# Optimization experiments

Hardware: AMD Instinct MI355X
Metric: run time of the kernel (lower is better)

## Reference

```python
import jax, jax.numpy as jnp
import numpy as np

EMBED_DIM = 1024
NUM_HEADS = 16
D_K = EMBED_DIM // NUM_HEADS


def setup_inputs() -> dict:
    key = jax.random.key(0)
    ks = jax.random.split(key, 9)
    s = 1.0 / np.sqrt(EMBED_DIM)
    x = jax.random.normal(ks[0], (4, 2048, EMBED_DIM), dtype=jnp.float32)
    # nn.Linear weights stored as [out, in]; we keep [in, out] for x @ W
    W_q = jax.random.uniform(ks[1], (EMBED_DIM, EMBED_DIM), jnp.float32, -s, s)
    b_q = jax.random.uniform(ks[2], (EMBED_DIM,), jnp.float32, -s, s)
    W_k = jax.random.uniform(ks[3], (EMBED_DIM, EMBED_DIM), jnp.float32, -s, s)
    b_k = jax.random.uniform(ks[4], (EMBED_DIM,), jnp.float32, -s, s)
    W_v = jax.random.uniform(ks[5], (EMBED_DIM, EMBED_DIM), jnp.float32, -s, s)
    b_v = jax.random.uniform(ks[6], (EMBED_DIM,), jnp.float32, -s, s)
    W_o = jax.random.uniform(ks[7], (EMBED_DIM, EMBED_DIM), jnp.float32, -s, s)
    b_o = jax.random.uniform(ks[8], (EMBED_DIM,), jnp.float32, -s, s)
    return {"x": x, "W_q": W_q, "b_q": b_q, "W_k": W_k, "b_k": b_k,
            "W_v": W_v, "b_v": b_v, "W_o": W_o, "b_o": b_o}


def reference(x, W_q, b_q, W_k, b_k, W_v, b_v, W_o, b_o):
    B, N, _ = x.shape
    # QKV projections, split into heads: [B, H, N, d_k]
    def proj(W, b):
        return (x @ W + b).reshape(B, N, NUM_HEADS, D_K).transpose(0, 2, 1, 3)
    Q, K, V = proj(W_q, b_q), proj(W_k, b_k), proj(W_v, b_v)
    scale = 1.0 / np.sqrt(D_K).astype(np.float32)
    scores = jnp.einsum('bhqd,bhkd->bhqk', Q, K) * scale  # [B,H,N,N]
    weights = jax.nn.softmax(scores, axis=-1)
    # dropout is identity in eval mode
    attn = jnp.einsum('bhqk,bhkd->bhqd', weights, V)  # [B,H,N,d_k]
    attn = attn.transpose(0, 2, 1, 3).reshape(B, N, EMBED_DIM)
    return attn @ W_o + b_o
```

## Files before the change

kernel.cpp:

```cpp
#include <hip/hip_runtime.h>

typedef __bf16 bf16;
typedef __attribute__((ext_vector_type(8))) __bf16 bf16x8;
typedef __attribute__((ext_vector_type(4))) __bf16 bf16x4;
typedef __attribute__((ext_vector_type(4))) float f32x4;

static __device__ __forceinline__ f32x4 mfma16(bf16x8 a, bf16x8 b, f32x4 c) {
    return __builtin_amdgcn_mfma_f32_16x16x32_bf16(a, b, c, 0, 0, 0);
}

static __device__ __forceinline__ void gll16(const bf16* g, bf16* l) {
    __builtin_amdgcn_global_load_lds(
        (const __attribute__((address_space(1))) unsigned int*)g,
        (__attribute__((address_space(3))) unsigned int*)l, 16, 0, 0);
}

__global__ __launch_bounds__(256) void prep_kernel(
    const float* __restrict__ x, bf16* __restrict__ xb,
    const float* __restrict__ Wq, const float* __restrict__ Wk,
    const float* __restrict__ Wv, const float* __restrict__ Wo,
    bf16* __restrict__ WTqkv, bf16* __restrict__ WTo,
    const float* __restrict__ bq, const float* __restrict__ bk,
    const float* __restrict__ bv, float* __restrict__ bcat)
{
    __shared__ bf16 tile[64][65];
    const int bid = blockIdx.x;
    const int tid = threadIdx.x;

    if (bid < 4096) {
        size_t i = ((size_t)bid * 256 + tid) * 8;
        float4 a0 = *(const float4*)&x[i];
        float4 a1 = *(const float4*)&x[i + 4];
        bf16x8 v = {(bf16)a0.x, (bf16)a0.y, (bf16)a0.z, (bf16)a0.w,
                    (bf16)a1.x, (bf16)a1.y, (bf16)a1.z, (bf16)a1.w};
        *(bf16x8*)&xb[i] = v;
    } else if (bid < 5120) {
        const int wb = bid - 4096;
        const int mi = wb >> 8;
        const int t  = wb & 255;
        const int tr = t >> 4;
        const int tc = t & 15;
        const float* src = (mi == 0) ? Wq : (mi == 1) ? Wk : (mi == 2) ? Wv : Wo;
        bf16* dst = (mi < 3) ? (WTqkv + (size_t)mi * 1024 * 1024) : WTo;

        #pragma unroll
        for (int i = 0; i < 16; i++) {
            int idx = i * 256 + tid;
            int rl = idx >> 6, cl = idx & 63;
            tile[rl][cl] = (bf16)src[(size_t)(tr * 64 + rl) * 1024 + tc * 64 + cl];
        }
        __syncthreads();
        #pragma unroll
        for (int i = 0; i < 16; i++) {
            int idx = i * 256 + tid;
            int rl = idx >> 6, cl = idx & 63;
            dst[(size_t)(tc * 64 + rl) * 1024 + tr * 64 + cl] = tile[cl][rl];
        }
    } else {
        int i = (bid - 5120) * 256 + tid;
        if (i < 1024) bcat[i] = bq[i];
        else if (i < 2048) bcat[i] = bk[i - 1024];
        else if (i < 3072) bcat[i] = bv[i - 2048];
    }
}

#define QSCALE 0.18033688011112043f
__global__ __launch_bounds__(256) void gemm_bf16_kernel(
    const bf16* __restrict__ A, const bf16* __restrict__ BT,
    const float* __restrict__ bias, bf16* __restrict__ C,
    int M, int N, int K, int scaleQ)
{
    __shared__ bf16 sA[2][128 * 32];
    __shared__ bf16 sB[2][128 * 32];
    const int tid  = threadIdx.x;
    const int lane = tid & 63;
    const int wave = tid >> 6;
    const int quad = lane >> 4;
    const int l15  = lane & 15;
    const int wm = (wave >> 1) * 64;
    const int wn = (wave & 1) * 64;
    const int m0 = blockIdx.y * 128;
    const int n0 = blockIdx.x * 128;

    const f32x4 fzero = {0.f, 0.f, 0.f, 0.f};
    f32x4 acc[4][4];
    #pragma unroll
    for (int i = 0; i < 4; i++)
        #pragma unroll
        for (int j = 0; j < 4; j++) acc[i][j] = fzero;

    float bv[4];
    #pragma unroll
    for (int nc = 0; nc < 4; nc++) bv[nc] = bias[n0 + wn + nc * 16 + l15];

    const int rA = lane >> 2;
    const int cAsw = ((lane & 3) ^ ((lane >> 3) & 3)) * 8;
    const int gsw = (l15 >> 1) & 3;

#define GSTAGE(K0, BUF)                                                           \
    _Pragma("unroll")                                                             \
    for (int p = 0; p < 2; p++) {                                                 \
        int r16 = (wave * 2 + p) * 16;                                            \
        gll16(&A[(size_t)(m0 + r16 + rA) * K + (K0) + cAsw], &sA[BUF][r16 * 32]); \
        gll16(&BT[(size_t)(n0 + r16 + rA) * K + (K0) + cAsw], &sB[BUF][r16 * 32]);\
    }

#define GCOMPUTE(BUF)                                                             \
    {                                                                             \
        bf16x8 aF[4], bF[4];                                                      \
        _Pragma("unroll")                                                         \
        for (int mc = 0; mc < 4; mc++)                                            \
            aF[mc] = *(const bf16x8*)&sA[BUF][(wm + mc * 16 + l15) * 32 + ((quad ^ gsw) * 8)]; \
        _Pragma("unroll")                                                         \
        for (int nc = 0; nc < 4; nc++)                                            \
            bF[nc] = *(const bf16x8*)&sB[BUF][(wn + nc * 16 + l15) * 32 + ((quad ^ gsw) * 8)]; \
        _Pragma("unroll")                                                         \
        for (int mc = 0; mc < 4; mc++)                                            \
            _Pragma("unroll")                                                     \
            for (int nc = 0; nc < 4; nc++)                                        \
                acc[mc][nc] = mfma16(aF[mc], bF[nc], acc[mc][nc]);                \
    }

    GSTAGE(0, 0);
    __syncthreads();
    int buf = 0;
    for (int k0 = 0; k0 < K - 32; k0 += 32, buf ^= 1) {
        GSTAGE(k0 + 32, buf ^ 1);
        __builtin_amdgcn_sched_barrier(0);
        GCOMPUTE(buf);
        __syncthreads();
    }
    GCOMPUTE(buf);

    const float sc = (scaleQ && n0 < 1024) ? QSCALE : 1.0f;
    #pragma unroll
    for (int mc = 0; mc < 4; mc++) {
        #pragma unroll
        for (int reg = 0; reg < 4; reg++) {
            int row = m0 + wm + mc * 16 + quad * 4 + reg;
            size_t base = (size_t)row * N + n0 + wn;
            #pragma unroll
            for (int nc = 0; nc < 4; nc++)
                C[base + nc * 16 + l15] = (bf16)((acc[mc][nc][reg] + bv[nc]) * sc);
        }
    }
}

__global__ __launch_bounds__(256) void gemm_bf16_f32out_kernel(
    const bf16* __restrict__ A, const bf16* __restrict__ BT,
    const float* __restrict__ bias, float* __restrict__ C,
    int M, int N, int K)
{
    __shared__ bf16 sA[2][128 * 32];
    __shared__ bf16 sB[2][128 * 32];
    const int tid  = threadIdx.x;
    const int lane = tid & 63;
    const int wave = tid >> 6;
    const int quad = lane >> 4;
    const int l15  = lane & 15;
    const int wm = (wave >> 1) * 64;
    const int wn = (wave & 1) * 64;
    const int m0 = blockIdx.y * 128;
    const int n0 = blockIdx.x * 128;

    const f32x4 fzero = {0.f, 0.f, 0.f, 0.f};
    f32x4 acc[4][4];
    #pragma unroll
    for (int i = 0; i < 4; i++)
        #pragma unroll
        for (int j = 0; j < 4; j++) acc[i][j] = fzero;

    float bv[4];
    #pragma unroll
    for (int nc = 0; nc < 4; nc++) bv[nc] = bias[n0 + wn + nc * 16 + l15];

    const int rA = lane >> 2;
    const int cAsw = ((lane & 3) ^ ((lane >> 3) & 3)) * 8;
    const int gsw = (l15 >> 1) & 3;

    GSTAGE(0, 0);
    __syncthreads();
    int buf = 0;
    for (int k0 = 0; k0 < K - 32; k0 += 32, buf ^= 1) {
        GSTAGE(k0 + 32, buf ^ 1);
        __builtin_amdgcn_sched_barrier(0);
        GCOMPUTE(buf);
        __syncthreads();
    }
    GCOMPUTE(buf);

#undef GSTAGE
#undef GCOMPUTE

    #pragma unroll
    for (int mc = 0; mc < 4; mc++) {
        #pragma unroll
        for (int reg = 0; reg < 4; reg++) {
            int row = m0 + wm + mc * 16 + quad * 4 + reg;
            size_t base = (size_t)row * N + n0 + wn;
            #pragma unroll
            for (int nc = 0; nc < 4; nc++)
                C[base + nc * 16 + l15] = acc[mc][nc][reg] + bv[nc];
        }
    }
}

__global__ __launch_bounds__(256) void vtrans_kernel(
    const bf16* __restrict__ QKVp, bf16* __restrict__ Vt)
{
    __shared__ bf16 tile[64][65];
    const int bid = blockIdx.x;
    const int bh = bid >> 5;
    const int nt = bid & 31;
    const int b = bh >> 4, h = bh & 15;
    const int tid = threadIdx.x;

    #pragma unroll
    for (int i = 0; i < 16; i++) {
        int idx = i * 256 + tid;
        int rl = idx >> 6, cl = idx & 63;
        tile[rl][cl] = QKVp[(size_t)(b * 2048 + nt * 64 + rl) * 3072 + 2048 + h * 64 + cl];
    }
    __syncthreads();
    #pragma unroll
    for (int i = 0; i < 16; i++) {
        int idx = i * 256 + tid;
        int rl = idx >> 6, cl = idx & 63;
        Vt[((size_t)bh * 64 + rl) * 2048 + nt * 64 + cl] = tile[cl][rl];
    }
}

__global__ __launch_bounds__(128, 2) void attn_kernel(
    const bf16* __restrict__ QKV, const bf16* __restrict__ Vt,
    bf16* __restrict__ Opre)
{
    __shared__ bf16 sK[2][64 * 64];
    __shared__ bf16 sV[2][64 * 64];

    const int tid  = threadIdx.x;
    const int lane = tid & 63;
    const int w    = tid >> 6;
    const int quad = lane >> 4;
    const int l15  = lane & 15;
    const int bid = (blockIdx.x & 7) * 128 + (blockIdx.x >> 3);
    const int bh = bid >> 4;
    const int qt = bid & 15;
    const int b = bh >> 4, h = bh & 15;
    const int q0 = qt * 128;

    bf16x8 qF[4][2];
    #pragma unroll
    for (int g = 0; g < 4; g++) {
        size_t qrow = (size_t)(b * 2048 + q0 + w * 64 + g * 16 + l15) * 3072 + h * 64;
        qF[g][0] = *(const bf16x8*)&QKV[qrow + quad * 8];
        qF[g][1] = *(const bf16x8*)&QKV[qrow + 32 + quad * 8];
    }

    const f32x4 fzero = {0.f, 0.f, 0.f, 0.f};
    const bf16 one = (bf16)1.0f;
    const bf16x8 ones = {one, one, one, one, one, one, one, one};
    f32x4 ps[4] = {fzero, fzero, fzero, fzero};
    f32x4 o[4][4];
    #pragma unroll
    for (int g = 0; g < 4; g++)
        #pragma unroll
        for (int mt = 0; mt < 4; mt++) o[g][mt] = fzero;

    const int srow = tid >> 3, sseg = tid & 7;
    const size_t kbase = (size_t)(b * 2048) * 3072 + 1024 + h * 64;
    const size_t vbase = (size_t)bh * 64 * 2048;
    const int sgsw = sseg ^ ((srow & 3) | (((srow >> 3) & 1) << 2));

    const int swk = (l15 & 3) | (((l15 >> 2) & 1) << 2);
    const int swv = (l15 & 3) | (((l15 >> 3) & 1) << 2);

    bf16x8 stK[4], stV[4];

#define ISSUE(KEY0)                                                               \
    _Pragma("unroll")                                                             \
    for (int p = 0; p < 4; p++) {                                                 \
        int row = srow + p * 16;                                                  \
        stK[p] = *(const bf16x8*)&QKV[kbase + (size_t)((KEY0) + row) * 3072 + sseg * 8]; \
        stV[p] = *(const bf16x8*)&Vt[vbase + (size_t)row * 2048 + (KEY0) + sseg * 8];    \
    }

#define COMMIT(BUF)                                                               \
    _Pragma("unroll")                                                             \
    for (int p = 0; p < 4; p++) {                                                 \
        int row = srow + p * 16;                                                  \
        *(bf16x8*)&sK[BUF][row * 64 + sgsw * 8] = stK[p];                         \
        *(bf16x8*)&sV[BUF][row * 64 + sgsw * 8] = stV[p];                         \
    }

    auto compute_tile = [&](const bf16* sKc, const bf16* sVc) {
        bf16x8 pB[4][2];
        __builtin_amdgcn_s_setprio(1);
        #pragma unroll
        for (int c = 0; c < 2; c++) {
            int kr = ((l15 >> 2) << 3) + (c << 2) + (l15 & 3);
            bf16x8 kA0 = *(const bf16x8*)&sKc[kr * 64 + ((quad ^ swk) * 8)];
            bf16x8 kA1 = *(const bf16x8*)&sKc[kr * 64 + (((4 + quad) ^ swk) * 8)];
            #pragma unroll
            for (int g = 0; g < 4; g++) {
                f32x4 st = mfma16(kA0, qF[g][0], fzero);
                st = mfma16(kA1, qF[g][1], st);
                #pragma unroll
                for (int r = 0; r < 4; r++) {
                    float p = __builtin_amdgcn_exp2f(st[r]);
                    pB[g][0][c * 4 + r] = (bf16)p;
                }
            }
        }
        bf16x8 vA0[4];
        #pragma unroll
        for (int mt = 0; mt < 4; mt++)
            vA0[mt] = *(const bf16x8*)&sVc[(mt * 16 + l15) * 64 + ((quad ^ swv) * 8)];
        #pragma unroll
        for (int c = 0; c < 2; c++) {
            int kr = ((l15 >> 2) << 3) + (c << 2) + (l15 & 3) + 32;
            bf16x8 kA0 = *(const bf16x8*)&sKc[kr * 64 + ((quad ^ swk) * 8)];
            bf16x8 kA1 = *(const bf16x8*)&sKc[kr * 64 + (((4 + quad) ^ swk) * 8)];
            #pragma unroll
            for (int g = 0; g < 4; g++) {
                f32x4 st = mfma16(kA0, qF[g][0], fzero);
                st = mfma16(kA1, qF[g][1], st);
                #pragma unroll
                for (int r = 0; r < 4; r++) {
                    float p = __builtin_amdgcn_exp2f(st[r]);
                    pB[g][1][c * 4 + r] = (bf16)p;
                }
            }
        }
        #pragma unroll
        for (int g = 0; g < 4; g++) ps[g] = mfma16(ones, pB[g][0], ps[g]);
        #pragma unroll
        for (int mt = 0; mt < 4; mt++)
            #pragma unroll
            for (int g = 0; g < 4; g++)
                o[g][mt] = mfma16(vA0[mt], pB[g][0], o[g][mt]);
        bf16x8 vA1[4];
        #pragma unroll
        for (int mt = 0; mt < 4; mt++)
            vA1[mt] = *(const bf16x8*)&sVc[(mt * 16 + l15) * 64 + (((4 + quad) ^ swv) * 8)];
        #pragma unroll
        for (int g = 0; g < 4; g++) ps[g] = mfma16(ones, pB[g][1], ps[g]);
        #pragma unroll
        for (int mt = 0; mt < 4; mt++)
            #pragma unroll
            for (int g = 0; g < 4; g++)
                o[g][mt] = mfma16(vA1[mt], pB[g][1], o[g][mt]);
        __builtin_amdgcn_s_setprio(0);
    };

    ISSUE(0);
    COMMIT(0);
    __syncthreads();

    for (int t = 0; t < 31; t++) {
        ISSUE((t + 1) * 64);
        __builtin_amdgcn_sched_barrier(0);
        compute_tile(sK[t & 1], sV[t & 1]);
        COMMIT((t + 1) & 1);
        __syncthreads();
    }
    compute_tile(sK[1], sV[1]);

#undef ISSUE
#undef COMMIT

    #pragma unroll
    for (int g = 0; g < 4; g++) {
        float inv = 1.0f / ps[g][0];
        size_t obase = (size_t)(b * 2048 + q0 + w * 64 + g * 16 + l15) * 1024 + h * 64;
        #pragma unroll
        for (int mt = 0; mt < 4; mt++) {
            bf16x4 ov = {(bf16)(o[g][mt][0] * inv), (bf16)(o[g][mt][1] * inv),
                         (bf16)(o[g][mt][2] * inv), (bf16)(o[g][mt][3] * inv)};
            *(bf16x4*)&Opre[obase + mt * 16 + quad * 4] = ov;
        }
    }
}

extern "C" void kernel_launch(void* const* d_in, const int* in_sizes, int n_in,
                              void* d_out, int out_size, void* d_ws, size_t ws_size,
                              hipStream_t stream)
{
    const float* x  = (const float*)d_in[0];
    const float* Wq = (const float*)d_in[1];
    const float* bq = (const float*)d_in[2];
    const float* Wk = (const float*)d_in[3];
    const float* bk = (const float*)d_in[4];
    const float* Wv = (const float*)d_in[5];
    const float* bv = (const float*)d_in[6];
    const float* Wo = (const float*)d_in[7];
    const float* bo = (const float*)d_in[8];
    float* out = (float*)d_out;

    bf16* WTqkv = (bf16*)d_ws;
    bf16* WTo   = WTqkv + (size_t)3072 * 1024;
    float* bcat = (float*)(WTo + (size_t)1024 * 1024);
    bf16* QKVp  = (bf16*)(bcat + 4096);
    bf16* Vt    = QKVp + (size_t)8192 * 3072;
    bf16* Apre  = Vt + (size_t)64 * 64 * 2048;
    bf16* xb    = Apre;
    (void)ws_size; (void)n_in; (void)in_sizes; (void)out_size;

    prep_kernel<<<5132, 256, 0, stream>>>(x, xb, Wq, Wk, Wv, Wo, WTqkv, WTo,
                                          bq, bk, bv, bcat);
    gemm_bf16_kernel<<<dim3(24, 64), 256, 0, stream>>>(xb, WTqkv, bcat, QKVp, 8192, 3072, 1024, 1);
    vtrans_kernel<<<2048, 256, 0, stream>>>(QKVp, Vt);
    attn_kernel<<<1024, 128, 0, stream>>>(QKVp, Vt, Apre);
    gemm_bf16_f32out_kernel<<<dim3(8, 64), 256, 0, stream>>>(Apre, WTo, bo, out, 8192, 1024, 1024);
}
```

Baseline: 269.0 us.

## Software-pipeline QK^T and PV across tiles with direct global-to-LDS loads

```diff
diff --git a/kernel.cpp b/kernel.cpp
--- a/kernel.cpp
+++ b/kernel.cpp
@@ -274,99 +274,96 @@
     const int swk = (l15 & 3) | (((l15 >> 2) & 1) << 2);
     const int swv = (l15 & 3) | (((l15 >> 3) & 1) << 2);
 
-    bf16x8 stK[4], stV[4];
-
-#define ISSUE(KEY0)                                                               \
+    bf16x8 pAr[4][2], pBr[4][2];
+    bf16x8 vA[4][2];
+
+#define STAGE(KEY0, BUF)                                                          \
     _Pragma("unroll")                                                             \
     for (int p = 0; p < 4; p++) {                                                 \
         int row = srow + p * 16;                                                  \
-        stK[p] = *(const bf16x8*)&QKV[kbase + (size_t)((KEY0) + row) * 3072 + sseg * 8]; \
-        stV[p] = *(const bf16x8*)&Vt[vbase + (size_t)row * 2048 + (KEY0) + sseg * 8];    \
-    }
-
-#define COMMIT(BUF)                                                               \
-    _Pragma("unroll")                                                             \
-    for (int p = 0; p < 4; p++) {                                                 \
-        int row = srow + p * 16;                                                  \
-        *(bf16x8*)&sK[BUF][row * 64 + sgsw * 8] = stK[p];                         \
-        *(bf16x8*)&sV[BUF][row * 64 + sgsw * 8] = stV[p];                         \
-    }
-
-    auto compute_tile = [&](const bf16* sKc, const bf16* sVc) {
-        bf16x8 pB[4][2];
+        gll16(&QKV[kbase + (size_t)((KEY0) + row) * 3072 + sgsw * 8],             \
+              &sK[BUF][(w * 8 + p * 16) * 64]);                                   \
+        gll16(&Vt[vbase + (size_t)row * 2048 + (KEY0) + sgsw * 8],                \
+              &sV[BUF][(w * 8 + p * 16) * 64]);                                   \
+    }
+
+#define VREAD(SV)                                                                 \
+    _Pragma("unroll")                                                             \
+    for (int mt = 0; mt < 4; mt++) {                                              \
+        vA[mt][0] = *(const bf16x8*)&(SV)[(mt * 16 + l15) * 64 + ((quad ^ swv) * 8)];       \
+        vA[mt][1] = *(const bf16x8*)&(SV)[(mt * 16 + l15) * 64 + (((4 + quad) ^ swv) * 8)]; \
+    }
+
+#define QKT(PB, SK)                                                               \
+    _Pragma("unroll")                                                             \
+    for (int ch = 0; ch < 2; ch++) {                                              \
+        _Pragma("unroll")                                                         \
+        for (int c = 0; c < 2; c++) {                                             \
+            int kr = ((l15 >> 2) << 3) + (c << 2) + (l15 & 3) + ch * 32;          \
+            bf16x8 kA0 = *(const bf16x8*)&(SK)[kr * 64 + ((quad ^ swk) * 8)];     \
+            bf16x8 kA1 = *(const bf16x8*)&(SK)[kr * 64 + (((4 + quad) ^ swk) * 8)];\
+            _Pragma("unroll")                                                     \
+            for (int g = 0; g < 4; g++) {                                         \
+                f32x4 st = mfma16(kA0, qF[g][0], fzero);                          \
+                st = mfma16(kA1, qF[g][1], st);                                   \
+                _Pragma("unroll")                                                 \
+                for (int r = 0; r < 4; r++)                                       \
+                    PB[g][ch][c * 4 + r] = (bf16)__builtin_amdgcn_exp2f(st[r]);   \
+            }                                                                     \
+        }                                                                         \
+    }
+
+#define PVACC(PA)                                                                 \
+    _Pragma("unroll")                                                             \
+    for (int g = 0; g < 4; g++) {                                                 \
+        ps[g] = mfma16(ones, PA[g][0], ps[g]);                                    \
+        ps[g] = mfma16(ones, PA[g][1], ps[g]);                                    \
+    }                                                                             \
+    _Pragma("unroll")                                                             \
+    for (int mt = 0; mt < 4; mt++)                                                \
+        _Pragma("unroll")                                                         \
+        for (int g = 0; g < 4; g++) {                                             \
+            o[g][mt] = mfma16(vA[mt][0], PA[g][0], o[g][mt]);                     \
+            o[g][mt] = mfma16(vA[mt][1], PA[g][1], o[g][mt]);                     \
+        }
+
+    STAGE(0, 0);
+    __syncthreads();
+    QKT(pAr, sK[0]);
+    STAGE(64, 1);
+
+    for (int tt = 0; tt < 15; tt++) {
+        const int t = tt * 2;
+        VREAD(sV[0]);
+        __syncthreads();
+        STAGE((t + 2) * 64, 0);
+        __builtin_amdgcn_sched_barrier(0);
         __builtin_amdgcn_s_setprio(1);
-        #pragma unroll
-        for (int c = 0; c < 2; c++) {
-            int kr = ((l15 >> 2) << 3) + (c << 2) + (l15 & 3);
-            bf16x8 kA0 = *(const bf16x8*)&sKc[kr * 64 + ((quad ^ swk) * 8)];
-            bf16x8 kA1 = *(const bf16x8*)&sKc[kr * 64 + (((4 + quad) ^ swk) * 8)];
-            #pragma unroll
-            for (int g = 0; g < 4; g++) {
-                f32x4 st = mfma16(kA0, qF[g][0], fzero);
-                st = mfma16(kA1, qF[g][1], st);
-                #pragma unroll
-                for (int r = 0; r < 4; r++) {
-                    float p = __builtin_amdgcn_exp2f(st[r]);
-                    pB[g][0][c * 4 + r] = (bf16)p;
-                }
-            }
-        }
-        bf16x8 vA0[4];
-        #pragma unroll
-        for (int mt = 0; mt < 4; mt++)
-            vA0[mt] = *(const bf16x8*)&sVc[(mt * 16 + l15) * 64 + ((quad ^ swv) * 8)];
-        #pragma unroll
-        for (int c = 0; c < 2; c++) {
-            int kr = ((l15 >> 2) << 3) + (c << 2) + (l15 & 3) + 32;
-            bf16x8 kA0 = *(const bf16x8*)&sKc[kr * 64 + ((quad ^ swk) * 8)];
-            bf16x8 kA1 = *(const bf16x8*)&sKc[kr * 64 + (((4 + quad) ^ swk) * 8)];
-            #pragma unroll
-            for (int g = 0; g < 4; g++) {
-                f32x4 st = mfma16(kA0, qF[g][0], fzero);
-                st = mfma16(kA1, qF[g][1], st);
-                #pragma unroll
-                for (int r = 0; r < 4; r++) {
-                    float p = __builtin_amdgcn_exp2f(st[r]);
-                    pB[g][1][c * 4 + r] = (bf16)p;
-                }
-            }
-        }
-        #pragma unroll
-        for (int g = 0; g < 4; g++) ps[g] = mfma16(ones, pB[g][0], ps[g]);
-        #pragma unroll
-        for (int mt = 0; mt < 4; mt++)
-            #pragma unroll
-            for (int g = 0; g < 4; g++)
-                o[g][mt] = mfma16(vA0[mt], pB[g][0], o[g][mt]);
-        bf16x8 vA1[4];
-        #pragma unroll
-        for (int mt = 0; mt < 4; mt++)
-            vA1[mt] = *(const bf16x8*)&sVc[(mt * 16 + l15) * 64 + (((4 + quad) ^ swv) * 8)];
-        #pragma unroll
-        for (int g = 0; g < 4; g++) ps[g] = mfma16(ones, pB[g][1], ps[g]);
-        #pragma unroll
-        for (int mt = 0; mt < 4; mt++)
-            #pragma unroll
-            for (int g = 0; g < 4; g++)
-                o[g][mt] = mfma16(vA1[mt], pB[g][1], o[g][mt]);
+        QKT(pBr, sK[1]);
+        PVACC(pAr);
         __builtin_amdgcn_s_setprio(0);
-    };
-
-    ISSUE(0);
-    COMMIT(0);
+        VREAD(sV[1]);
+        __syncthreads();
+        STAGE((t + 3) * 64, 1);
+        __builtin_amdgcn_sched_barrier(0);
+        __builtin_amdgcn_s_setprio(1);
+        QKT(pAr, sK[0]);
+        PVACC(pBr);
+        __builtin_amdgcn_s_setprio(0);
+    }
+    VREAD(sV[0]);
     __syncthreads();
-
-    for (int t = 0; t < 31; t++) {
-        ISSUE((t + 1) * 64);
-        __builtin_amdgcn_sched_barrier(0);
-        compute_tile(sK[t & 1], sV[t & 1]);
-        COMMIT((t + 1) & 1);
-        __syncthreads();
-    }
-    compute_tile(sK[1], sV[1]);
-
-#undef ISSUE
-#undef COMMIT
+    __builtin_amdgcn_s_setprio(1);
+    QKT(pBr, sK[1]);
+    PVACC(pAr);
+    __builtin_amdgcn_s_setprio(0);
+    VREAD(sV[1]);
+    PVACC(pBr);
+
+#undef STAGE
+#undef VREAD
+#undef QKT
+#undef PVACC
 
     #pragma unroll
     for (int g = 0; g < 4; g++) {
```

After: 265.5 us. Within noise of the previous version (-1.3%).

## Rewrite QKV GEMM with 256-wide tiles, 8 waves, and fused V transpose

Applied to the files above, without the earlier changes.

```diff
diff --git a/kernel.cpp b/kernel.cpp
--- a/kernel.cpp
+++ b/kernel.cpp
@@ -65,22 +65,36 @@
 }
 
 #define QSCALE 0.18033688011112043f
-__global__ __launch_bounds__(256) void gemm_bf16_kernel(
+__global__ __launch_bounds__(512, 2) void gemm_qkv_kernel(
     const bf16* __restrict__ A, const bf16* __restrict__ BT,
     const float* __restrict__ bias, bf16* __restrict__ C,
-    int M, int N, int K, int scaleQ)
+    bf16* __restrict__ Vt)
 {
-    __shared__ bf16 sA[2][128 * 32];
-    __shared__ bf16 sB[2][128 * 32];
+    __shared__ bf16 sA[2 * 8192];
+    __shared__ bf16 sB[2 * 16384];
+
     const int tid  = threadIdx.x;
     const int lane = tid & 63;
     const int wave = tid >> 6;
+    const int wm   = wave >> 2;
+    const int wn   = wave & 3;
     const int quad = lane >> 4;
     const int l15  = lane & 15;
-    const int wm = (wave >> 1) * 64;
-    const int wn = (wave & 1) * 64;
+    const int gx   = l15 & 7;
     const int m0 = blockIdx.y * 128;
-    const int n0 = blockIdx.x * 128;
+    const int n0 = blockIdx.x * 256;
+    const int K = 1024;
+    const int N = 3072;
+
+    const int srow8 = lane >> 3;
+    const int scol  = ((lane & 7) ^ srow8) * 8;
+
+#define S_A(L, T)                                                                  \
+    gll16(&A[(size_t)(m0 + (L) * 64 + wave * 8 + srow8) * K + (T) * 64 + scol],    \
+          &sA[((T) & 1) * 8192 + ((L) * 64 + wave * 8) * 64])
+#define S_B(L, T)                                                                  \
+    gll16(&BT[(size_t)(n0 + (L) * 64 + wave * 8 + srow8) * K + (T) * 64 + scol],   \
+          &sB[((T) & 1) * 16384 + ((L) * 64 + wave * 8) * 64])
 
     const f32x4 fzero = {0.f, 0.f, 0.f, 0.f};
     f32x4 acc[4][4];
@@ -91,57 +105,132 @@
 
     float bv[4];
     #pragma unroll
-    for (int nc = 0; nc < 4; nc++) bv[nc] = bias[n0 + wn + nc * 16 + l15];
-
-    const int rA = lane >> 2;
-    const int cAsw = ((lane & 3) ^ ((lane >> 3) & 3)) * 8;
-    const int gsw = (l15 >> 1) & 3;
-
-#define GSTAGE(K0, BUF)                                                           \
-    _Pragma("unroll")                                                             \
-    for (int p = 0; p < 2; p++) {                                                 \
-        int r16 = (wave * 2 + p) * 16;                                            \
-        gll16(&A[(size_t)(m0 + r16 + rA) * K + (K0) + cAsw], &sA[BUF][r16 * 32]); \
-        gll16(&BT[(size_t)(n0 + r16 + rA) * K + (K0) + cAsw], &sB[BUF][r16 * 32]);\
-    }
-
-#define GCOMPUTE(BUF)                                                             \
-    {                                                                             \
-        bf16x8 aF[4], bF[4];                                                      \
-        _Pragma("unroll")                                                         \
-        for (int mc = 0; mc < 4; mc++)                                            \
-            aF[mc] = *(const bf16x8*)&sA[BUF][(wm + mc * 16 + l15) * 32 + ((quad ^ gsw) * 8)]; \
-        _Pragma("unroll")                                                         \
-        for (int nc = 0; nc < 4; nc++)                                            \
-            bF[nc] = *(const bf16x8*)&sB[BUF][(wn + nc * 16 + l15) * 32 + ((quad ^ gsw) * 8)]; \
-        _Pragma("unroll")                                                         \
-        for (int mc = 0; mc < 4; mc++)                                            \
-            _Pragma("unroll")                                                     \
-            for (int nc = 0; nc < 4; nc++)                                        \
-                acc[mc][nc] = mfma16(aF[mc], bF[nc], acc[mc][nc]);                \
-    }
-
-    GSTAGE(0, 0);
-    __syncthreads();
-    int buf = 0;
-    for (int k0 = 0; k0 < K - 32; k0 += 32, buf ^= 1) {
-        GSTAGE(k0 + 32, buf ^ 1);
+    for (int cf = 0; cf < 4; cf++) bv[cf] = bias[n0 + wn * 64 + cf * 16 + l15];
+
+    bf16x8 aF[4][2], bF[2][2];
+
+#define PH0(CB)                                                                    \
+    {                                                                              \
+        _Pragma("unroll")                                                          \
+        for (int mc = 0; mc < 4; mc++)                                             \
+            _Pragma("unroll")                                                      \
+            for (int ks = 0; ks < 2; ks++)                                         \
+                aF[mc][ks] = *(const bf16x8*)&sA[(CB) * 8192 +                     \
+                    (wm * 64 + mc * 16 + l15) * 64 + (((ks * 4 + quad) ^ gx) * 8)];\
+        _Pragma("unroll")                                                          \
+        for (int nc = 0; nc < 2; nc++)                                             \
+            _Pragma("unroll")                                                      \
+            for (int ks = 0; ks < 2; ks++)                                         \
+                bF[nc][ks] = *(const bf16x8*)&sB[(CB) * 16384 +                    \
+                    (wn * 64 + nc * 16 + l15) * 64 + (((ks * 4 + quad) ^ gx) * 8)];\
+        __builtin_amdgcn_s_barrier();                                              \
+        __builtin_amdgcn_s_setprio(1);                                             \
+        _Pragma("unroll")                                                          \
+        for (int mc = 0; mc < 4; mc++)                                             \
+            _Pragma("unroll")                                                      \
+            for (int nc = 0; nc < 2; nc++)                                         \
+                _Pragma("unroll")                                                  \
+                for (int ks = 0; ks < 2; ks++)                                     \
+                    acc[mc][nc] = mfma16(aF[mc][ks], bF[nc][ks], acc[mc][nc]);     \
+        __builtin_amdgcn_s_setprio(0);                                             \
+        __builtin_amdgcn_s_barrier();                                              \
+    }
+
+#define PH1(CB)                                                                    \
+    {                                                                              \
+        _Pragma("unroll")                                                          \
+        for (int nc = 0; nc < 2; nc++)                                             \
+            _Pragma("unroll")                                                      \
+            for (int ks = 0; ks < 2; ks++)                                         \
+                bF[nc][ks] = *(const bf16x8*)&sB[(CB) * 16384 +                    \
+                    (wn * 64 + 32 + nc * 16 + l15) * 64 +                          \
+                    (((ks * 4 + quad) ^ gx) * 8)];                                 \
+        __builtin_amdgcn_s_barrier();                                              \
+        __builtin_amdgcn_s_setprio(1);                                             \
+        _Pragma("unroll")                                                          \
+        for (int mc = 0; mc < 4; mc++)                                             \
+            _Pragma("unroll")                                                      \
+            for (int nc = 0; nc < 2; nc++)                                         \
+                _Pragma("unroll")                                                  \
+                for (int ks = 0; ks < 2; ks++)                                     \
+                    acc[mc][2 + nc] = mfma16(aF[mc][ks], bF[nc][ks], acc[mc][2 + nc]); \
+        __builtin_amdgcn_s_setprio(0);                                             \
+        __builtin_amdgcn_s_barrier();                                              \
+    }
+
+    S_A(0, 0); S_A(1, 0);
+    S_B(0, 0); S_B(1, 0); S_B(2, 0); S_B(3, 0);
+    S_A(0, 1); S_A(1, 1);
+    asm volatile("s_waitcnt vmcnt(2)" ::: "memory");
+    __builtin_amdgcn_s_barrier();
+
+    for (int i = 0; i < 14; ++i) {
+        const int cb = i & 1;
+        S_B(0, i + 1); S_B(1, i + 1);
         __builtin_amdgcn_sched_barrier(0);
-        GCOMPUTE(buf);
+        PH0(cb);
+        S_B(2, i + 1); S_B(3, i + 1);
+        __builtin_amdgcn_sched_barrier(0);
+        PH1(cb);
+        S_A(0, i + 2); S_A(1, i + 2);
+        asm volatile("s_waitcnt vmcnt(2)" ::: "memory");
+        __builtin_amdgcn_s_barrier();
+    }
+    S_B(0, 15); S_B(1, 15);
+    __builtin_amdgcn_sched_barrier(0);
+    PH0(0);
+    S_B(2, 15); S_B(3, 15);
+    __builtin_amdgcn_sched_barrier(0);
+    PH1(0);
+    asm volatile("s_waitcnt vmcnt(0)" ::: "memory");
+    __builtin_amdgcn_s_barrier();
+    PH0(1);
+    PH1(1);
+
+#undef S_A
+#undef S_B
+#undef PH0
+#undef PH1
+
+    if (n0 >= 2048) {
         __syncthreads();
-    }
-    GCOMPUTE(buf);
-
-    const float sc = (scaleQ && n0 < 1024) ? QSCALE : 1.0f;
-    #pragma unroll
-    for (int mc = 0; mc < 4; mc++) {
-        #pragma unroll
-        for (int reg = 0; reg < 4; reg++) {
-            int row = m0 + wm + mc * 16 + quad * 4 + reg;
-            size_t base = (size_t)row * N + n0 + wn;
-            #pragma unroll
-            for (int nc = 0; nc < 4; nc++)
-                C[base + nc * 16 + l15] = (bf16)((acc[mc][nc][reg] + bv[nc]) * sc);
+        #pragma unroll
+        for (int mc = 0; mc < 4; mc++)
+            #pragma unroll
+            for (int cf = 0; cf < 4; cf++) {
+                int col = wn * 64 + cf * 16 + l15;
+                int row = wm * 64 + mc * 16 + quad * 4;
+                bf16x4 v = {(bf16)(acc[mc][cf][0] + bv[cf]),
+                            (bf16)(acc[mc][cf][1] + bv[cf]),
+                            (bf16)(acc[mc][cf][2] + bv[cf]),
+                            (bf16)(acc[mc][cf][3] + bv[cf])};
+                *(bf16x4*)&sB[col * 128 + (row ^ ((col & 15) << 3))] = v;
+            }
+        __syncthreads();
+        const int b = m0 >> 11, mloc = m0 & 2047;
+        const int hp = (n0 - 2048) >> 6;
+        #pragma unroll
+        for (int it = 0; it < 16; it++) {
+            int chunk = it * 512 + tid;
+            int col = chunk >> 5;
+            int tok = (chunk & 31) * 4;
+            bf16x4 v = *(const bf16x4*)&sB[col * 128 + (tok ^ ((col & 15) << 3))];
+            int habs = hp + (col >> 6);
+            int dd = col & 63;
+            *(bf16x4*)&Vt[((size_t)((b * 16 + habs) * 64 + dd)) * 2048 + mloc + tok] = v;
+        }
+    } else {
+        const float sc = (n0 < 1024) ? QSCALE : 1.0f;
+        #pragma unroll
+        for (int mc = 0; mc < 4; mc++) {
+            #pragma unroll
+            for (int reg = 0; reg < 4; reg++) {
+                int row = m0 + wm * 64 + mc * 16 + quad * 4 + reg;
+                size_t base = (size_t)row * N + n0 + wn * 64;
+                #pragma unroll
+                for (int cf = 0; cf < 4; cf++)
+                    C[base + cf * 16 + l15] = (bf16)((acc[mc][cf][reg] + bv[cf]) * sc);
+            }
         }
     }
 }
@@ -178,6 +267,30 @@
     const int cAsw = ((lane & 3) ^ ((lane >> 3) & 3)) * 8;
     const int gsw = (l15 >> 1) & 3;
 
+#define GSTAGE(K0, BUF)                                                           \
+    _Pragma("unroll")                                                             \
+    for (int p = 0; p < 2; p++) {                                                 \
+        int r16 = (wave * 2 + p) * 16;                                            \
+        gll16(&A[(size_t)(m0 + r16 + rA) * K + (K0) + cAsw], &sA[BUF][r16 * 32]); \
+        gll16(&BT[(size_t)(n0 + r16 + rA) * K + (K0) + cAsw], &sB[BUF][r16 * 32]);\
+    }
+
+#define GCOMPUTE(BUF)                                                             \
+    {                                                                             \
+        bf16x8 aF[4], bF[4];                                                      \
+        _Pragma("unroll")                                                         \
+        for (int mc = 0; mc < 4; mc++)                                            \
+            aF[mc] = *(const bf16x8*)&sA[BUF][(wm + mc * 16 + l15) * 32 + ((quad ^ gsw) * 8)]; \
+        _Pragma("unroll")                                                         \
+        for (int nc = 0; nc < 4; nc++)                                            \
+            bF[nc] = *(const bf16x8*)&sB[BUF][(wn + nc * 16 + l15) * 32 + ((quad ^ gsw) * 8)]; \
+        _Pragma("unroll")                                                         \
+        for (int mc = 0; mc < 4; mc++)                                            \
+            _Pragma("unroll")                                                     \
+            for (int nc = 0; nc < 4; nc++)                                        \
+                acc[mc][nc] = mfma16(aF[mc], bF[nc], acc[mc][nc]);                \
+    }
+
     GSTAGE(0, 0);
     __syncthreads();
     int buf = 0;
@@ -202,31 +315,6 @@
             for (int nc = 0; nc < 4; nc++)
                 C[base + nc * 16 + l15] = acc[mc][nc][reg] + bv[nc];
         }
-    }
-}
-
-__global__ __launch_bounds__(256) void vtrans_kernel(
-    const bf16* __restrict__ QKVp, bf16* __restrict__ Vt)
-{
-    __shared__ bf16 tile[64][65];
-    const int bid = blockIdx.x;
-    const int bh = bid >> 5;
-    const int nt = bid & 31;
-    const int b = bh >> 4, h = bh & 15;
-    const int tid = threadIdx.x;
-
-    #pragma unroll
-    for (int i = 0; i < 16; i++) {
-        int idx = i * 256 + tid;
-        int rl = idx >> 6, cl = idx & 63;
-        tile[rl][cl] = QKVp[(size_t)(b * 2048 + nt * 64 + rl) * 3072 + 2048 + h * 64 + cl];
-    }
-    __syncthreads();
-    #pragma unroll
-    for (int i = 0; i < 16; i++) {
-        int idx = i * 256 + tid;
-        int rl = idx >> 6, cl = idx & 63;
-        Vt[((size_t)bh * 64 + rl) * 2048 + nt * 64 + cl] = tile[cl][rl];
     }
 }
 
@@ -407,8 +495,7 @@
 
     prep_kernel<<<5132, 256, 0, stream>>>(x, xb, Wq, Wk, Wv, Wo, WTqkv, WTo,
                                           bq, bk, bv, bcat);
-    gemm_bf16_kernel<<<dim3(24, 64), 256, 0, stream>>>(xb, WTqkv, bcat, QKVp, 8192, 3072, 1024, 1);
-    vtrans_kernel<<<2048, 256, 0, stream>>>(QKVp, Vt);
+    gemm_qkv_kernel<<<dim3(12, 64), 512, 0, stream>>>(xb, WTqkv, bcat, QKVp, Vt);
     attn_kernel<<<1024, 128, 0, stream>>>(QKVp, Vt, Apre);
     gemm_bf16_f32out_kernel<<<dim3(8, 64), 256, 0, stream>>>(Apre, WTo, bo, out, 8192, 1024, 1024);
 }
```

Result: slower. 286.4 us (+6.5%).
